# Optimization experiments

Hardware: AMD Instinct MI355X
Metric: run time of the kernel (lower is better)

The kernel has to match this reference:

```python
import jax, jax.numpy as jnp
import numpy as np

EMBED_DIM = 1024
NUM_HEADS = 16
HEAD_DIM = EMBED_DIM // NUM_HEADS
SCALE = EMBED_DIM ** (-0.5)  # NOTE: module scales by embed_dim**-0.5, not head_dim**-0.5


def setup_inputs() -> dict:
    key = jax.random.key(0)
    ks = jax.random.split(key, 10)
    B, N = 2, 2048
    q = jax.random.normal(ks[0], (B, N, EMBED_DIM), dtype=jnp.float32)
    kv = jax.random.normal(ks[1], (B, N, EMBED_DIM), dtype=jnp.float32)
    mask = jax.random.randint(ks[2], (B, N), 0, 2, dtype=jnp.int64)
    s = 0.02
    Wq = jax.random.normal(ks[3], (EMBED_DIM, EMBED_DIM), dtype=jnp.float32) * s
    bq = jax.random.normal(ks[4], (EMBED_DIM,), dtype=jnp.float32) * s
    Wkv = jax.random.normal(ks[5], (EMBED_DIM, 2 * EMBED_DIM), dtype=jnp.float32) * s
    bkv = jax.random.normal(ks[6], (2 * EMBED_DIM,), dtype=jnp.float32) * s
    Wo = jax.random.normal(ks[7], (EMBED_DIM, EMBED_DIM), dtype=jnp.float32) * s
    bo = jax.random.normal(ks[8], (EMBED_DIM,), dtype=jnp.float32) * s
    return {"q": q, "kv": kv, "mask": mask, "Wq": Wq, "bq": bq,
            "Wkv": Wkv, "bkv": bkv, "Wo": Wo, "bo": bo}


def _softmax_plus_one(x):
    # softmax with +1 in the denominator; max clipped at 0, no grad through max
    m = jax.lax.stop_gradient(jnp.maximum(jnp.max(x, axis=-1, keepdims=True), 0.0))
    unnorm = jnp.exp(x - m)
    denom = jnp.sum(unnorm, axis=-1, keepdims=True) + jnp.exp(-m)
    return unnorm / denom


def _split_heads(x):
    b, n, _ = x.shape
    return x.reshape(b, n, NUM_HEADS, HEAD_DIM).transpose(0, 2, 1, 3)  # b h n d


def reference(q, kv, mask, Wq, bq, Wkv, bkv, Wo, bo):
    xq = q @ Wq + bq
    xkv = kv @ Wkv + bkv
    xk, xv = jnp.split(xkv, 2, axis=-1)
    xq, xk, xv = _split_heads(xq), _split_heads(xk), _split_heads(xv)
    logits = jnp.einsum('bhnd,bhmd->bhnm', xq * SCALE, xk)
    # prepare_mask: log of 0/1 mask broadcast over (head, query) dims
    logmask = jnp.log(mask.astype(logits.dtype))[:, None, None, :]
    logits = logits + logmask
    # attn_dropout = 0.0 -> no-op
    scores = _softmax_plus_one(logits)  # add_one_to_softmax=True
    attn = jnp.einsum('bhnm,bhmd->bhnd', scores, xv)
    b, h, n, d = attn.shape
    out = attn.transpose(0, 2, 1, 3).reshape(b, n, h * d)
    return out @ Wo + bo
```

## Files before the change

### kernel.cpp

```cpp
#include <hip/hip_runtime.h>
#include <hip/hip_bf16.h>

static constexpr int CB = 2, CN = 2048, CE = 1024, CH = 16, CD = 64;
static constexpr int CM = CB * CN;
#define SCALE_Q (1.4426950408889634f / 32.0f)

typedef __attribute__((ext_vector_type(8))) short short8;
typedef __attribute__((ext_vector_type(4))) float f32x4;
typedef __attribute__((ext_vector_type(16))) float f32x16;
typedef __attribute__((ext_vector_type(4))) float f4;
typedef __attribute__((ext_vector_type(4))) unsigned short u16x4;

#define MFMA16(a, b, c) __builtin_amdgcn_mfma_f32_16x16x32_bf16((a), (b), (c), 0, 0, 0)
#define MFMA32(a, b, c) __builtin_amdgcn_mfma_f32_32x32x16_bf16((a), (b), (c), 0, 0, 0)

static __device__ __forceinline__ unsigned short f2bf(float f) {
  union { __hip_bfloat16 h; unsigned short u; } cv;
  cv.h = __float2bfloat16(f);
  return cv.u;
}
static __device__ __forceinline__ unsigned int pk2bf(float lo, float hi) {
  return (unsigned int)f2bf(lo) | ((unsigned int)f2bf(hi) << 16);
}

typedef unsigned int u32;
static __device__ __forceinline__ void gload16(const void* g, void* l) {
  __builtin_amdgcn_global_load_lds(
      (const __attribute__((address_space(1))) u32*)g,
      (__attribute__((address_space(3))) u32*)l, 16, 0, 0);
}

#define SYNC_L()                                                 \
  do {                                                           \
    asm volatile("s_waitcnt lgkmcnt(0)" ::: "memory");           \
    __builtin_amdgcn_s_barrier();                                \
    __builtin_amdgcn_sched_barrier(0);                           \
  } while (0)

__global__ __launch_bounds__(256) void prep(
    const float* __restrict__ Wq, const float* __restrict__ Wkv,
    const float* __restrict__ Wo, unsigned short* __restrict__ WqT,
    unsigned short* __restrict__ WkvT, unsigned short* __restrict__ WoT,
    const int* __restrict__ mask, int* __restrict__ cidx, int* __restrict__ cnt) {
  __shared__ float tile[32][33];
  __shared__ int tsum[256];
  const int bid = blockIdx.x;
  const int t = threadIdx.x;
  if (bid < 4096) {
    const float* in; unsigned short* out; int C, tb;
    if (bid < 1024)      { in = Wq;  out = WqT;  C = 1024; tb = bid; }
    else if (bid < 3072) { in = Wkv; out = WkvT; C = 2048; tb = bid - 1024; }
    else                 { in = Wo;  out = WoT;  C = 1024; tb = bid - 3072; }
    const int R = 1024;
    int tc = C >> 5;
    int bc = tb % tc, br = tb / tc;
    int c = t & 31, r0 = t >> 5;
#pragma unroll
    for (int i = 0; i < 4; ++i) {
      int r = r0 + i * 8;
      tile[r][c] = in[(size_t)(br * 32 + r) * C + bc * 32 + c];
    }
    __syncthreads();
#pragma unroll
    for (int i = 0; i < 4; ++i) {
      int r = r0 + i * 8;
      out[(size_t)(bc * 32 + r) * R + br * 32 + c] = f2bf(tile[c][r]);
    }
  } else {
    const int b = bid - 4096;
    int m[8], s = 0;
#pragma unroll
    for (int i = 0; i < 8; ++i) {
      m[i] = mask[b * CN + t * 8 + i] != 0;
      s += m[i];
    }
    tsum[t] = s;
    __syncthreads();
    if (t == 0) {
      int acc = 0;
      for (int i = 0; i < 256; ++i) { int v = tsum[i]; tsum[i] = acc; acc += v; }
      cnt[b] = acc;
    }
    __syncthreads();
    int pos = tsum[t];
#pragma unroll
    for (int i = 0; i < 8; ++i)
      if (m[i]) cidx[b * CN + pos++] = t * 8 + i;
  }
}

template <bool AF32, bool OUT_BF16, bool VSPLIT, bool GATHER>
static __device__ __forceinline__ void gemm_body(
    char* lds, int bm, int bn,
    const void* __restrict__ Ap, const unsigned short* __restrict__ Bt,
    const float* __restrict__ bias, void* __restrict__ C0,
    unsigned short* __restrict__ C1, int N, int K, float outscale,
    const int* __restrict__ cidx, const int* __restrict__ cnt) {
  constexpr int ASTR = AF32 ? 72 : 64;
  unsigned short* As = (unsigned short*)lds;
  char* Bs = lds + 2 * 64 * ASTR * 2;
  const int m0 = bm << 6, n0 = bn << 7;

  if constexpr (GATHER) {
    const int bb = m0 >> 11;
    const int ru = min((cnt[bb] + 63) & ~63, CN);
    if ((m0 & 2047) >= ru) return;
  }

  const int t = threadIdx.x;
  const int lane = t & 63, w = t >> 6;
  const int wr = w >> 1, wc = w & 1;
  const int fr = lane & 15, fg = lane >> 4;

  const int sw8 = (t & 7) ^ ((t >> 3) & 7);

  const int ach = t & 3;
  size_t arow;
  {
    int gr = m0 + (t >> 2);
    if constexpr (GATHER) {
      int bb = gr >> 11, r = gr & 2047;
      int cb_ = cnt[bb];
      int cr = r < cb_ ? r : (cb_ > 0 ? cb_ - 1 : 0);
      gr = bb * CN + cidx[bb * CN + cr];
    }
    arow = (size_t)gr * K;
  }

  f32x4 acc[2][4];
#pragma unroll
  for (int i = 0; i < 2; ++i)
#pragma unroll
    for (int j = 0; j < 4; ++j) acc[i][j] = (f32x4){0.f, 0.f, 0.f, 0.f};

  f4 a0, a1, a2, a3;
  auto ALOAD = [&](int k0) {
    const float* src = (const float*)Ap + arow + k0 + ach * 8;
    a0 = *(const f4*)src;
    a1 = *(const f4*)(src + 4);
    a2 = *(const f4*)(src + 32);
    a3 = *(const f4*)(src + 36);
  };
  auto AWRITE = [&](int bi) {
    short8 av0, av1;
#pragma unroll
    for (int j = 0; j < 4; ++j) {
      av0[j] = (short)f2bf(a0[j]);
      av0[4 + j] = (short)f2bf(a1[j]);
      av1[j] = (short)f2bf(a2[j]);
      av1[4 + j] = (short)f2bf(a3[j]);
    }
    unsigned short* dst = As + bi * 64 * ASTR + (t >> 2) * ASTR;
    *(short8*)&dst[ach * 8] = av0;
    *(short8*)&dst[32 + ach * 8] = av1;
  };
  auto BSTAGE = [&](int bi, int k0) {
#pragma unroll
    for (int i = 0; i < 4; ++i) {
      int s = t + i * 256;
      gload16(Bt + (size_t)(n0 + (s >> 3)) * K + k0 + sw8 * 8,
              Bs + bi * 128 * 128 + s * 16);
    }
    if constexpr (!AF32) {
#pragma unroll
      for (int i = 0; i < 2; ++i) {
        int s = t + i * 256;
        gload16((const unsigned short*)Ap + (size_t)(m0 + (s >> 3)) * K + k0 + sw8 * 8,
                (char*)As + bi * 64 * 128 + s * 16);
      }
    }
  };

  if constexpr (AF32) { ALOAD(0); AWRITE(0); }
  BSTAGE(0, 0);
  __syncthreads();

  const int nt = K >> 6;
  int buf = 0;
  for (int tt = 0; tt < nt; ++tt) {
    const bool np = tt < nt - 1;
    if (np) {
      if constexpr (AF32) ALOAD((tt + 1) << 6);
      BSTAGE(buf ^ 1, (tt + 1) << 6);
    }
    if (np) {
      if constexpr (AF32) asm volatile("s_waitcnt vmcnt(8)" ::: "memory");
      else                asm volatile("s_waitcnt vmcnt(6)" ::: "memory");
    } else {
      asm volatile("s_waitcnt vmcnt(0)" ::: "memory");
    }
    __builtin_amdgcn_s_barrier();
    __builtin_amdgcn_sched_barrier(0);

    short8 af[2][2], bfv[4][2];
#pragma unroll
    for (int mi = 0; mi < 2; ++mi) {
      const int r = wr * 32 + mi * 16 + fr;
#pragma unroll
      for (int kk = 0; kk < 2; ++kk) {
        if constexpr (AF32) {
          af[mi][kk] = *(const short8*)&As[buf * 64 * ASTR + r * ASTR + kk * 32 + fg * 8];
        } else {
          const int sl = (kk * 4 + fg) ^ (r & 7);
          af[mi][kk] = *(const short8*)((char*)As + buf * 64 * 128 + r * 128 + sl * 16);
        }
      }
    }
#pragma unroll
    for (int ni = 0; ni < 4; ++ni) {
      const int r = wc * 64 + ni * 16 + fr;
#pragma unroll
      for (int kk = 0; kk < 2; ++kk) {
        const int sl = (kk * 4 + fg) ^ (r & 7);
        bfv[ni][kk] = *(const short8*)(Bs + buf * 128 * 128 + r * 128 + sl * 16);
      }
    }
#pragma unroll
    for (int kk = 0; kk < 2; ++kk)
#pragma unroll
      for (int mi = 0; mi < 2; ++mi)
#pragma unroll
        for (int ni = 0; ni < 4; ++ni)
          acc[mi][ni] = MFMA16(af[mi][kk], bfv[ni][kk], acc[mi][ni]);

    if (np) {
      if constexpr (AF32) AWRITE(buf ^ 1);
    }
    SYNC_L();
    buf ^= 1;
  }

#pragma unroll
  for (int mi = 0; mi < 2; ++mi) {
    int row0 = m0 + wr * 32 + mi * 16 + fg * 4;
#pragma unroll
    for (int ni = 0; ni < 4; ++ni) {
      int col = n0 + wc * 64 + ni * 16 + fr;
      float bv = bias[col];
      if constexpr (VSPLIT) {
        if (col < CE) {
#pragma unroll
          for (int rr = 0; rr < 4; ++rr)
            ((unsigned short*)C0)[(size_t)(row0 + rr) * CE + col] =
                f2bf((acc[mi][ni][rr] + bv) * outscale);
        } else {
          u16x4 pk;
#pragma unroll
          for (int rr = 0; rr < 4; ++rr) pk[rr] = f2bf((acc[mi][ni][rr] + bv) * outscale);
          int b = row0 / CN, n = row0 % CN;
          *(u16x4*)&C1[((size_t)b * CE + (col - CE)) * CN + n] = pk;
        }
      } else if constexpr (OUT_BF16) {
#pragma unroll
        for (int rr = 0; rr < 4; ++rr)
          ((unsigned short*)C0)[(size_t)(row0 + rr) * N + col] =
              f2bf((acc[mi][ni][rr] + bv) * outscale);
      } else {
#pragma unroll
        for (int rr = 0; rr < 4; ++rr)
          ((float*)C0)[(size_t)(row0 + rr) * N + col] = (acc[mi][ni][rr] + bv) * outscale;
      }
    }
  }
}

__global__ __launch_bounds__(256) void gemm_qkv(
    const float* __restrict__ q, const unsigned short* __restrict__ WqT,
    const float* __restrict__ bq, unsigned short* __restrict__ xq,
    const float* __restrict__ kv, const unsigned short* __restrict__ WkvT,
    const float* __restrict__ bkv, unsigned short* __restrict__ xk,
    unsigned short* __restrict__ xvT,
    const int* __restrict__ cidx, const int* __restrict__ cnt) {
  __shared__ char lds[2 * 64 * 72 * 2 + 2 * 128 * 128];
  const int raw = blockIdx.x;
  if (raw < 512) {
    const int k = raw & 7, j = raw >> 3;
    gemm_body<true, true, false, false>(lds, k + 8 * (j >> 3), j & 7, q, WqT,
                                        bq, xq, nullptr, CE, CE, SCALE_Q,
                                        nullptr, nullptr);
  } else {
    const int r2 = raw - 512;
    const int k = r2 & 7, j = r2 >> 3;
    gemm_body<true, true, true, true>(lds, k + 8 * (j >> 4), j & 15, kv, WkvT,
                                      bkv, xk, xvT, 2 * CE, CE, 1.0f, cidx, cnt);
  }
}

__global__ __launch_bounds__(256) void gemm_o(
    const unsigned short* __restrict__ attnA, const unsigned short* __restrict__ WoT,
    const float* __restrict__ bo, float* __restrict__ out) {
  __shared__ char lds[2 * 64 * 128 + 2 * 128 * 128];
  const int k = blockIdx.x & 7, j = blockIdx.x >> 3;
  gemm_body<false, false, false, false>(lds, k + 8 * (j >> 3), j & 7,
                                        attnA, WoT, bo, out, nullptr, CE, CE,
                                        1.0f, nullptr, nullptr);
}

__global__ __launch_bounds__(256, 2) void attn_fwd(
    unsigned short* __restrict__ xq,
    const unsigned short* __restrict__ xk,
    const unsigned short* __restrict__ xvT,
    const int* __restrict__ cnt) {
  __shared__ unsigned short Kt[64][72];
  __shared__ unsigned short Vt[64][72];
  __shared__ float dsh[4][32];

  const int bid = blockIdx.x;
  const int qblk = bid & 15;
  const int h = (bid >> 4) & 15;
  const int b = bid >> 8;
  const int t = threadIdx.x, lane = t & 63, w = t >> 6;
  const int l31 = lane & 31, h5 = lane >> 5;
  const int q0 = qblk * 128 + w * 32;

  const int cntb = cnt[b];
  const int nt = (cntb + 63) >> 6;

  short8 qf[4];
  {
    const unsigned short* qp =
        xq + ((size_t)(b * CN + q0 + l31)) * CE + h * CD + h5 * 8;
#pragma unroll
    for (int dk = 0; dk < 4; ++dk) qf[dk] = *(const short8*)(qp + dk * 16);
  }

  f32x16 o[2];
#pragma unroll
  for (int c = 0; c < 2; ++c)
#pragma unroll
    for (int i = 0; i < 16; ++i) o[c][i] = 0.f;
  float ls = 0.f;

  const int r0s = t >> 3, sl0 = t & 7;
  const int r1s = r0s + 32, sl1 = sl0;

  short8 rk[2], rv[2];
  if (nt > 0) {
    rk[0] = *(const short8*)(xk + ((size_t)(b * CN + r0s)) * CE + h * CD + sl0 * 8);
    rk[1] = *(const short8*)(xk + ((size_t)(b * CN + r1s)) * CE + h * CD + sl1 * 8);
    rv[0] = *(const short8*)(xvT + ((size_t)(b * CE + h * CD + r0s)) * CN + sl0 * 8);
    rv[1] = *(const short8*)(xvT + ((size_t)(b * CE + h * CD + r1s)) * CN + sl1 * 8);
  }

  for (int kt = 0; kt < nt; ++kt) {
    __syncthreads();
    *(short8*)&Kt[r0s][sl0 * 8] = rk[0];
    *(short8*)&Kt[r1s][sl1 * 8] = rk[1];
    *(short8*)&Vt[r0s][sl0 * 8] = rv[0];
    *(short8*)&Vt[r1s][sl1 * 8] = rv[1];
    __syncthreads();

    if (kt < nt - 1) {
      const int kn = (kt + 1) * 64;
      rk[0] = *(const short8*)(xk + ((size_t)(b * CN + kn + r0s)) * CE + h * CD + sl0 * 8);
      rk[1] = *(const short8*)(xk + ((size_t)(b * CN + kn + r1s)) * CE + h * CD + sl1 * 8);
      rv[0] = *(const short8*)(xvT + ((size_t)(b * CE + h * CD + r0s)) * CN + kn + sl0 * 8);
      rv[1] = *(const short8*)(xvT + ((size_t)(b * CE + h * CD + r1s)) * CN + kn + sl1 * 8);
    }

    short8 ka[2][4];
#pragma unroll
    for (int cb = 0; cb < 2; ++cb)
#pragma unroll
      for (int dk = 0; dk < 4; ++dk)
        ka[cb][dk] = *(const short8*)&Kt[cb * 32 + l31][(dk * 2 + h5) * 8];

    f32x16 s2[2];
#pragma unroll
    for (int cb = 0; cb < 2; ++cb) {
#pragma unroll
      for (int i = 0; i < 16; ++i) s2[cb][i] = 0.f;
#pragma unroll
      for (int dk = 0; dk < 4; ++dk)
        s2[cb] = MFMA32(ka[cb][dk], qf[dk], s2[cb]);
    }

    const bool tail = (kt == nt - 1) && (cntb & 63);
    unsigned int U[2][4][2];
#pragma unroll
    for (int cb = 0; cb < 2; ++cb) {
      float p[16];
#pragma unroll
      for (int i = 0; i < 16; ++i) {
        float sv = s2[cb][i];
        if (tail) {
          int cpos = kt * 64 + cb * 32 + (i & 3) + 8 * (i >> 2) + 4 * h5;
          sv = (cpos < cntb) ? sv : -30000.f;
        }
        p[i] = __builtin_amdgcn_exp2f(sv);
        ls += p[i];
      }
#pragma unroll
      for (int m = 0; m < 4; ++m) {
        U[cb][m][0] = pk2bf(p[4 * m], p[4 * m + 1]);
        U[cb][m][1] = pk2bf(p[4 * m + 2], p[4 * m + 3]);
      }
    }

    short8 vb[2][4];
#pragma unroll
    for (int nb = 0; nb < 2; ++nb)
#pragma unroll
      for (int kc = 0; kc < 4; ++kc)
        vb[nb][kc] = *(const short8*)&Vt[nb * 32 + l31][(kc * 2 + h5) * 8];

#pragma unroll
    for (int kc = 0; kc < 4; ++kc) {
      const int cb = kc >> 1, k2 = (kc & 1) * 2;
      unsigned int su0 = h5 ? U[cb][k2 + 1][0] : U[cb][k2][0];
      unsigned int su1 = h5 ? U[cb][k2 + 1][1] : U[cb][k2][1];
      unsigned int st0 = h5 ? U[cb][k2][0] : U[cb][k2 + 1][0];
      unsigned int st1 = h5 ? U[cb][k2][1] : U[cb][k2 + 1][1];
      unsigned int x0 = (unsigned int)__shfl_xor((int)st0, 32);
      unsigned int x1 = (unsigned int)__shfl_xor((int)st1, 32);
      union { unsigned int u[4]; short8 v; } pa;
      pa.u[0] = h5 ? x0 : su0;
      pa.u[1] = h5 ? x1 : su1;
      pa.u[2] = h5 ? su0 : x0;
      pa.u[3] = h5 ? su1 : x1;
#pragma unroll
      for (int nb = 0; nb < 2; ++nb)
        o[nb] = MFMA32(pa.v, vb[nb][kc], o[nb]);
    }
  }

  {
    float tot = ls + __shfl_xor(ls, 32);
    if (h5 == 0) dsh[w][l31] = 1.0f / (tot + 1.0f);
  }
  __syncthreads();
#pragma unroll
  for (int m = 0; m < 4; ++m) {
    f4 dn4 = *(const f4*)&dsh[w][m * 8 + h5 * 4];
#pragma unroll
    for (int rr = 0; rr < 4; ++rr) {
      int q = m * 8 + h5 * 4 + rr;
      size_t row = (size_t)(b * CN + q0 + q);
#pragma unroll
      for (int nb = 0; nb < 2; ++nb) {
        float val = o[nb][m * 4 + rr] * dn4[rr];
        xq[row * CE + h * CD + nb * 32 + l31] = f2bf(val);
      }
    }
  }
}

extern "C" void kernel_launch(void* const* d_in, const int* in_sizes, int n_in,
                              void* d_out, int out_size, void* d_ws, size_t ws_size,
                              hipStream_t stream) {
  const float* q    = (const float*)d_in[0];
  const float* kv   = (const float*)d_in[1];
  const int*   mask = (const int*)d_in[2];
  const float* Wq   = (const float*)d_in[3];
  const float* bq   = (const float*)d_in[4];
  const float* Wkv  = (const float*)d_in[5];
  const float* bkv  = (const float*)d_in[6];
  const float* Wo   = (const float*)d_in[7];
  const float* bo   = (const float*)d_in[8];
  (void)in_sizes; (void)n_in; (void)out_size; (void)ws_size;

  char* ws = (char*)d_ws;
  unsigned short* WoT  = (unsigned short*)(ws);
  unsigned short* xq   = (unsigned short*)(ws + (2u  << 20));
  unsigned short* xk   = (unsigned short*)(ws + (10u << 20));
  unsigned short* xvT  = (unsigned short*)(ws + (18u << 20));
  unsigned short* WqT  = (unsigned short*)(ws + (26u << 20));
  unsigned short* WkvT = (unsigned short*)(ws + (28u << 20));
  int*            cidx = (int*)(ws + (32u << 20));
  int*            cnt  = (int*)(ws + (32u << 20) + 16384);

  prep<<<4098, 256, 0, stream>>>(Wq, Wkv, Wo, WqT, WkvT, WoT, mask, cidx, cnt);

  gemm_qkv<<<1536, 256, 0, stream>>>(q, WqT, bq, xq, kv, WkvT, bkv, xk, xvT, cidx, cnt);

  attn_fwd<<<CB * CH * 16, 256, 0, stream>>>(xq, xk, xvT, cnt);

  gemm_o<<<512, 256, 0, stream>>>(xq, WoT, bo, (float*)d_out);
}
```

Before: 96.71 us.

## Enlarge GEMM tiles to 128x128 with 512-thread blocks and swizzled A staging

The QKV and output GEMMs move from 64x128 tiles with 256 threads to 128x128 tiles with 512 threads, halving the grid sizes. The fp32-converted A tile now goes into LDS with the same XOR swizzle as the bf16 path, replacing the padded stride, and the vmcnt waits are adjusted to the smaller number of loads per thread. The aim is more reuse of each loaded B tile and fewer blocks overall. The cost is more LDS per block and a launch bound of 4 blocks per CU, which may cap registers and cause spills. It also leaves fewer blocks to spread across the CUs.

Result: slower. 99.00 us (+2.4%).

```diff
diff --git a/kernel.cpp b/kernel.cpp
--- a/kernel.cpp
+++ b/kernel.cpp
@@ -96,10 +96,10 @@
     const float* __restrict__ bias, void* __restrict__ C0,
     unsigned short* __restrict__ C1, int N, int K, float outscale,
     const int* __restrict__ cidx, const int* __restrict__ cnt) {
-  constexpr int ASTR = AF32 ? 72 : 64;
-  unsigned short* As = (unsigned short*)lds;
-  char* Bs = lds + 2 * 64 * ASTR * 2;
-  const int m0 = bm << 6, n0 = bn << 7;
+  constexpr int TB = 16384;
+  char* As = lds;
+  char* Bs = lds + 2 * TB;
+  const int m0 = bm << 7, n0 = bn << 7;
 
   if constexpr (GATHER) {
     const int bb = m0 >> 11;
@@ -150,23 +150,24 @@
       av1[j] = (short)f2bf(a2[j]);
       av1[4 + j] = (short)f2bf(a3[j]);
     }
-    unsigned short* dst = As + bi * 64 * ASTR + (t >> 2) * ASTR;
-    *(short8*)&dst[ach * 8] = av0;
-    *(short8*)&dst[32 + ach * 8] = av1;
+    const int r = t >> 2;
+    char* dst = As + bi * TB + r * 128;
+    *(short8*)(dst + ((ach ^ (r & 7)) * 16)) = av0;
+    *(short8*)(dst + (((ach + 4) ^ (r & 7)) * 16)) = av1;
   };
   auto BSTAGE = [&](int bi, int k0) {
 #pragma unroll
-    for (int i = 0; i < 4; ++i) {
-      int s = t + i * 256;
+    for (int i = 0; i < 2; ++i) {
+      int s = t + i * 512;
       gload16(Bt + (size_t)(n0 + (s >> 3)) * K + k0 + sw8 * 8,
-              Bs + bi * 128 * 128 + s * 16);
+              Bs + bi * TB + s * 16);
     }
     if constexpr (!AF32) {
 #pragma unroll
       for (int i = 0; i < 2; ++i) {
-        int s = t + i * 256;
+        int s = t + i * 512;
         gload16((const unsigned short*)Ap + (size_t)(m0 + (s >> 3)) * K + k0 + sw8 * 8,
-                (char*)As + bi * 64 * 128 + s * 16);
+                As + bi * TB + s * 16);
       }
     }
   };
@@ -184,8 +185,8 @@
       BSTAGE(buf ^ 1, (tt + 1) << 6);
     }
     if (np) {
-      if constexpr (AF32) asm volatile("s_waitcnt vmcnt(8)" ::: "memory");
-      else                asm volatile("s_waitcnt vmcnt(6)" ::: "memory");
+      if constexpr (AF32) asm volatile("s_waitcnt vmcnt(6)" ::: "memory");
+      else                asm volatile("s_waitcnt vmcnt(4)" ::: "memory");
     } else {
       asm volatile("s_waitcnt vmcnt(0)" ::: "memory");
     }
@@ -198,12 +199,8 @@
       const int r = wr * 32 + mi * 16 + fr;
 #pragma unroll
       for (int kk = 0; kk < 2; ++kk) {
-        if constexpr (AF32) {
-          af[mi][kk] = *(const short8*)&As[buf * 64 * ASTR + r * ASTR + kk * 32 + fg * 8];
-        } else {
-          const int sl = (kk * 4 + fg) ^ (r & 7);
-          af[mi][kk] = *(const short8*)((char*)As + buf * 64 * 128 + r * 128 + sl * 16);
-        }
+        const int sl = (kk * 4 + fg) ^ (r & 7);
+        af[mi][kk] = *(const short8*)(As + buf * TB + r * 128 + sl * 16);
       }
     }
 #pragma unroll
@@ -212,7 +209,7 @@
 #pragma unroll
       for (int kk = 0; kk < 2; ++kk) {
         const int sl = (kk * 4 + fg) ^ (r & 7);
-        bfv[ni][kk] = *(const short8*)(Bs + buf * 128 * 128 + r * 128 + sl * 16);
+        bfv[ni][kk] = *(const short8*)(Bs + buf * TB + r * 128 + sl * 16);
       }
     }
 #pragma unroll
@@ -264,32 +261,32 @@
   }
 }
 
-__global__ __launch_bounds__(256) void gemm_qkv(
+__global__ __launch_bounds__(512, 4) void gemm_qkv(
     const float* __restrict__ q, const unsigned short* __restrict__ WqT,
     const float* __restrict__ bq, unsigned short* __restrict__ xq,
     const float* __restrict__ kv, const unsigned short* __restrict__ WkvT,
     const float* __restrict__ bkv, unsigned short* __restrict__ xk,
     unsigned short* __restrict__ xvT,
     const int* __restrict__ cidx, const int* __restrict__ cnt) {
-  __shared__ char lds[2 * 64 * 72 * 2 + 2 * 128 * 128];
+  __shared__ char lds[4 * 16384];
   const int raw = blockIdx.x;
-  if (raw < 512) {
+  if (raw < 256) {
     const int k = raw & 7, j = raw >> 3;
     gemm_body<true, true, false, false>(lds, k + 8 * (j >> 3), j & 7, q, WqT,
                                         bq, xq, nullptr, CE, CE, SCALE_Q,
                                         nullptr, nullptr);
   } else {
-    const int r2 = raw - 512;
+    const int r2 = raw - 256;
     const int k = r2 & 7, j = r2 >> 3;
     gemm_body<true, true, true, true>(lds, k + 8 * (j >> 4), j & 15, kv, WkvT,
                                       bkv, xk, xvT, 2 * CE, CE, 1.0f, cidx, cnt);
   }
 }
 
-__global__ __launch_bounds__(256) void gemm_o(
+__global__ __launch_bounds__(512, 4) void gemm_o(
     const unsigned short* __restrict__ attnA, const unsigned short* __restrict__ WoT,
     const float* __restrict__ bo, float* __restrict__ out) {
-  __shared__ char lds[2 * 64 * 128 + 2 * 128 * 128];
+  __shared__ char lds[4 * 16384];
   const int k = blockIdx.x & 7, j = blockIdx.x >> 3;
   gemm_body<false, false, false, false>(lds, k + 8 * (j >> 3), j & 7,
                                         attnA, WoT, bo, out, nullptr, CE, CE,
@@ -471,9 +468,9 @@
 
   prep<<<4098, 256, 0, stream>>>(Wq, Wkv, Wo, WqT, WkvT, WoT, mask, cidx, cnt);
 
-  gemm_qkv<<<1536, 256, 0, stream>>>(q, WqT, bq, xq, kv, WkvT, bkv, xk, xvT, cidx, cnt);
+  gemm_qkv<<<768, 512, 0, stream>>>(q, WqT, bq, xq, kv, WkvT, bkv, xk, xvT, cidx, cnt);
 
   attn_fwd<<<CB * CH * 16, 256, 0, stream>>>(xq, xk, xvT, cnt);
 
-  gemm_o<<<512, 256, 0, stream>>>(xq, WoT, bo, (float*)d_out);
-}
+  gemm_o<<<256, 512, 0, stream>>>(xq, WoT, bo, (float*)d_out);
+}
```

## Triple-buffer GEMM LDS stages with two-tile-ahead prefetch

Applied to the files above, without the earlier changes.

Converts the shared GEMM body from double to triple buffering in LDS, issuing global loads two K-tiles ahead instead of one. It uses two alternating register sets for the fp32 A operand and manually unrolls the loop by two. Wait counts are adjusted so each step only waits for the tile it needs. The aim is to hide more global-memory latency behind the MFMA work. In exchange it uses more LDS and more registers, which may lower occupancy.

Result: slower. 99.75 us (+3.2%).

```diff
diff --git a/kernel.cpp b/kernel.cpp
--- a/kernel.cpp
+++ b/kernel.cpp
@@ -30,12 +30,19 @@
       (__attribute__((address_space(3))) u32*)l, 16, 0, 0);
 }
 
+#define SYNC_V(NSTR)                                             \
+  do {                                                           \
+    asm volatile("s_waitcnt vmcnt(" NSTR ")" ::: "memory");      \
+    __builtin_amdgcn_s_barrier();                                \
+    __builtin_amdgcn_sched_barrier(0);                           \
+  } while (0)
 #define SYNC_L()                                                 \
   do {                                                           \
     asm volatile("s_waitcnt lgkmcnt(0)" ::: "memory");           \
     __builtin_amdgcn_s_barrier();                                \
     __builtin_amdgcn_sched_barrier(0);                           \
   } while (0)
+#define FENCE() __builtin_amdgcn_sched_barrier(0)
 
 __global__ __launch_bounds__(256) void prep(
     const float* __restrict__ Wq, const float* __restrict__ Wkv,
@@ -97,8 +104,9 @@
     unsigned short* __restrict__ C1, int N, int K, float outscale,
     const int* __restrict__ cidx, const int* __restrict__ cnt) {
   constexpr int ASTR = AF32 ? 72 : 64;
+  constexpr int ABYTES = 64 * ASTR * 2;
   unsigned short* As = (unsigned short*)lds;
-  char* Bs = lds + 2 * 64 * ASTR * 2;
+  char* Bs = lds + 3 * ABYTES;
   const int m0 = bm << 6, n0 = bn << 7;
 
   if constexpr (GATHER) {
@@ -133,64 +141,75 @@
 #pragma unroll
     for (int j = 0; j < 4; ++j) acc[i][j] = (f32x4){0.f, 0.f, 0.f, 0.f};
 
-  f4 a0, a1, a2, a3;
-  auto ALOAD = [&](int k0) {
+  auto BSTAGE = [&](int bi, int k0) {
+#pragma unroll
+    for (int i = 0; i < 4; ++i) {
+      int s = t + i * 256;
+      gload16(Bt + (size_t)(n0 + (s >> 3)) * K + k0 + sw8 * 8,
+              Bs + bi * 128 * 128 + s * 16);
+    }
+    if constexpr (!AF32) {
+#pragma unroll
+      for (int i = 0; i < 2; ++i) {
+        int s = t + i * 256;
+        gload16((const unsigned short*)Ap + (size_t)(m0 + (s >> 3)) * K + k0 + sw8 * 8,
+                (char*)As + bi * 64 * 128 + s * 16);
+      }
+    }
+  };
+
+  const int nt = K >> 6;
+  f4 sA0, sA1, sA2, sA3, sB0, sB1, sB2, sB3;
+
+  auto ALOAD_TO = [&](int k0, f4& r0, f4& r1, f4& r2, f4& r3) {
     const float* src = (const float*)Ap + arow + k0 + ach * 8;
-    a0 = *(const f4*)src;
-    a1 = *(const f4*)(src + 4);
-    a2 = *(const f4*)(src + 32);
-    a3 = *(const f4*)(src + 36);
+    r0 = *(const f4*)src;
+    r1 = *(const f4*)(src + 4);
+    r2 = *(const f4*)(src + 32);
+    r3 = *(const f4*)(src + 36);
   };
-  auto AWRITE = [&](int bi) {
+  auto AWRITE_FROM = [&](int bi, f4& r0, f4& r1, f4& r2, f4& r3) {
     short8 av0, av1;
 #pragma unroll
     for (int j = 0; j < 4; ++j) {
-      av0[j] = (short)f2bf(a0[j]);
-      av0[4 + j] = (short)f2bf(a1[j]);
-      av1[j] = (short)f2bf(a2[j]);
-      av1[4 + j] = (short)f2bf(a3[j]);
+      av0[j] = (short)f2bf(r0[j]);
+      av0[4 + j] = (short)f2bf(r1[j]);
+      av1[j] = (short)f2bf(r2[j]);
+      av1[4 + j] = (short)f2bf(r3[j]);
     }
     unsigned short* dst = As + bi * 64 * ASTR + (t >> 2) * ASTR;
     *(short8*)&dst[ach * 8] = av0;
     *(short8*)&dst[32 + ach * 8] = av1;
   };
-  auto BSTAGE = [&](int bi, int k0) {
-#pragma unroll
-    for (int i = 0; i < 4; ++i) {
-      int s = t + i * 256;
-      gload16(Bt + (size_t)(n0 + (s >> 3)) * K + k0 + sw8 * 8,
-              Bs + bi * 128 * 128 + s * 16);
-    }
-    if constexpr (!AF32) {
-#pragma unroll
-      for (int i = 0; i < 2; ++i) {
-        int s = t + i * 256;
-        gload16((const unsigned short*)Ap + (size_t)(m0 + (s >> 3)) * K + k0 + sw8 * 8,
-                (char*)As + bi * 64 * 128 + s * 16);
-      }
-    }
-  };
-
-  if constexpr (AF32) { ALOAD(0); AWRITE(0); }
+
+  if constexpr (AF32) {
+    ALOAD_TO(0, sA0, sA1, sA2, sA3);
+    AWRITE_FROM(0, sA0, sA1, sA2, sA3);
+  }
+  FENCE();
   BSTAGE(0, 0);
-  __syncthreads();
-
-  const int nt = K >> 6;
-  int buf = 0;
-  for (int tt = 0; tt < nt; ++tt) {
-    const bool np = tt < nt - 1;
-    if (np) {
-      if constexpr (AF32) ALOAD((tt + 1) << 6);
-      BSTAGE(buf ^ 1, (tt + 1) << 6);
-    }
-    if (np) {
-      if constexpr (AF32) asm volatile("s_waitcnt vmcnt(8)" ::: "memory");
-      else                asm volatile("s_waitcnt vmcnt(6)" ::: "memory");
+  FENCE();
+  if constexpr (AF32) ALOAD_TO(64, sB0, sB1, sB2, sB3);
+  FENCE();
+  BSTAGE(1, 64);
+  asm volatile("s_waitcnt lgkmcnt(0)" ::: "memory");
+
+  auto STEP = [&](int tt, f4& la0, f4& la1, f4& la2, f4& la3,
+                  f4& wa0, f4& wa1, f4& wa2, f4& wa3) {
+    const int cur = tt % 3;
+    const bool p2 = (tt + 2) < nt;
+    if (p2) {
+      if constexpr (AF32) ALOAD_TO((tt + 2) << 6, la0, la1, la2, la3);
+      FENCE();
+      BSTAGE((tt + 2) % 3, (tt + 2) << 6);
+    }
+    if (p2) {
+      if constexpr (AF32) SYNC_V("16"); else SYNC_V("12");
+    } else if (tt + 1 < nt) {
+      if constexpr (AF32) SYNC_V("8"); else SYNC_V("6");
     } else {
-      asm volatile("s_waitcnt vmcnt(0)" ::: "memory");
-    }
-    __builtin_amdgcn_s_barrier();
-    __builtin_amdgcn_sched_barrier(0);
+      SYNC_V("0");
+    }
 
     short8 af[2][2], bfv[4][2];
 #pragma unroll
@@ -199,10 +218,10 @@
 #pragma unroll
       for (int kk = 0; kk < 2; ++kk) {
         if constexpr (AF32) {
-          af[mi][kk] = *(const short8*)&As[buf * 64 * ASTR + r * ASTR + kk * 32 + fg * 8];
+          af[mi][kk] = *(const short8*)&As[cur * 64 * ASTR + r * ASTR + kk * 32 + fg * 8];
         } else {
           const int sl = (kk * 4 + fg) ^ (r & 7);
-          af[mi][kk] = *(const short8*)((char*)As + buf * 64 * 128 + r * 128 + sl * 16);
+          af[mi][kk] = *(const short8*)((char*)As + cur * 64 * 128 + r * 128 + sl * 16);
         }
       }
     }
@@ -212,7 +231,7 @@
 #pragma unroll
       for (int kk = 0; kk < 2; ++kk) {
         const int sl = (kk * 4 + fg) ^ (r & 7);
-        bfv[ni][kk] = *(const short8*)(Bs + buf * 128 * 128 + r * 128 + sl * 16);
+        bfv[ni][kk] = *(const short8*)(Bs + cur * 128 * 128 + r * 128 + sl * 16);
       }
     }
 #pragma unroll
@@ -223,11 +242,16 @@
         for (int ni = 0; ni < 4; ++ni)
           acc[mi][ni] = MFMA16(af[mi][kk], bfv[ni][kk], acc[mi][ni]);
 
-    if (np) {
-      if constexpr (AF32) AWRITE(buf ^ 1);
+    if (tt + 1 < nt) {
+      if constexpr (AF32)
+        AWRITE_FROM((tt + 1) % 3, wa0, wa1, wa2, wa3);
     }
     SYNC_L();
-    buf ^= 1;
+  };
+
+  for (int t2 = 0; t2 < nt; t2 += 2) {
+    STEP(t2,     sA0, sA1, sA2, sA3, sB0, sB1, sB2, sB3);
+    STEP(t2 + 1, sB0, sB1, sB2, sB3, sA0, sA1, sA2, sA3);
   }
 
 #pragma unroll
@@ -271,7 +295,7 @@
     const float* __restrict__ bkv, unsigned short* __restrict__ xk,
     unsigned short* __restrict__ xvT,
     const int* __restrict__ cidx, const int* __restrict__ cnt) {
-  __shared__ char lds[2 * 64 * 72 * 2 + 2 * 128 * 128];
+  __shared__ char lds[3 * 64 * 72 * 2 + 3 * 128 * 128];
   const int raw = blockIdx.x;
   if (raw < 512) {
     const int k = raw & 7, j = raw >> 3;
@@ -289,7 +313,7 @@
 __global__ __launch_bounds__(256) void gemm_o(
     const unsigned short* __restrict__ attnA, const unsigned short* __restrict__ WoT,
     const float* __restrict__ bo, float* __restrict__ out) {
-  __shared__ char lds[2 * 64 * 128 + 2 * 128 * 128];
+  __shared__ char lds[3 * 64 * 128 + 3 * 128 * 128];
   const int k = blockIdx.x & 7, j = blockIdx.x >> 3;
   gemm_body<false, false, false, false>(lds, k + 8 * (j >> 3), j & 7,
                                         attnA, WoT, bo, out, nullptr, CE, CE,
```
